# Optimization experiments

Hardware: AMD Instinct MI355X
Metric: run time of the kernel (lower is better)

The kernel has to match this reference:

```python
import jax, jax.numpy as jnp
import numpy as np

N_NODES = 50000
N_EDGES = 800000
IN_F, HID_F, OUT_F = 128, 128, 64


def setup_inputs() -> dict:
    key = jax.random.key(0)
    k1, k2, k3, k4, k5, k6 = jax.random.split(key, 6)
    edge_index = jax.random.randint(k1, (2, N_EDGES), 0, N_NODES, dtype=jnp.int64 if jax.config.jax_enable_x64 else jnp.int32)
    features = jax.random.normal(k2, (N_NODES, IN_F), dtype=jnp.float32)
    # GCNLayer weights (torch.randn init, no bias)
    W0 = jax.random.normal(k3, (IN_F, HID_F), dtype=jnp.float32)
    W1 = jax.random.normal(k4, (HID_F, HID_F), dtype=jnp.float32)
    # out_layer nn.Linear(hidden, out): weight [out, hid] used as x @ W.T + b; store transposed
    bound = 1.0 / np.sqrt(HID_F)
    W_out = jax.random.uniform(k5, (HID_F, OUT_F), minval=-bound, maxval=bound, dtype=jnp.float32)
    b_out = jax.random.uniform(k6, (OUT_F,), minval=-bound, maxval=bound, dtype=jnp.float32)
    return {"edge_index": edge_index, "features": features, "W0": W0, "W1": W1, "W_out": W_out, "b_out": b_out}


def _gcn_layer(edge_index, x, W):
    # support = x @ W ; out = A @ support ; A COO: rows=edge_index[0], cols=edge_index[1], vals=1
    support = x @ W                                   # [N, F_out]
    msgs = support[edge_index[1]]                      # gather per edge: [E, F_out]
    agg = jax.ops.segment_sum(msgs, edge_index[0], num_segments=N_NODES)  # scatter-add rows
    return jax.nn.relu(agg)


def reference(edge_index, features, W0, W1, W_out, b_out):
    x = _gcn_layer(edge_index, features, W0)
    x = _gcn_layer(edge_index, x, W1)
    return x @ W_out + b_out
```

## Files before the change

### kernel.cpp

```cpp
#include <hip/hip_runtime.h>

#define N_NODES 50000
#define N_EDGES 800000
#define SCAN_TILE 2048
#define SCAN_NBLK ((N_NODES + SCAN_TILE - 1) / SCAN_TILE)

template <int M, bool RELU_IN, bool BIAS>
__global__ __launch_bounds__(512) void gemm_k(const float* __restrict__ X,
                                              const float* __restrict__ W,
                                              const float* __restrict__ bias,
                                              float* __restrict__ Y) {
    constexpr int K = 128;
    constexpr int ROWS = 64;
    constexpr int XSTR = 136;

    __shared__ float wl[K * M];
    __shared__ float xl[ROWS * XSTR];

    const int tid = threadIdx.x;
    const int row0 = blockIdx.x * ROWS;

    {
        const float4* w4 = reinterpret_cast<const float4*>(W);
        float4* wl4 = reinterpret_cast<float4*>(wl);
        constexpr int TOT4 = K * M / 4;
        #pragma unroll
        for (int i = tid; i < TOT4; i += 512) wl4[i] = w4[i];
    }
    {
        const float4* x4 = reinterpret_cast<const float4*>(X);
        #pragma unroll
        for (int i = tid; i < ROWS * 32; i += 512) {
            const int r = i >> 5, c = i & 31;
            const int gr = row0 + r;
            float4 v = {0.f, 0.f, 0.f, 0.f};
            if (gr < N_NODES) v = x4[(size_t)gr * 32 + c];
            if (RELU_IN) {
                v.x = fmaxf(v.x, 0.f);
                v.y = fmaxf(v.y, 0.f);
                v.z = fmaxf(v.z, 0.f);
                v.w = fmaxf(v.w, 0.f);
            }
            reinterpret_cast<float4*>(&xl[r * XSTR])[c] = v;
        }
    }
    __syncthreads();

    constexpr int TPRG = M / 8;
    constexpr int NRG = 512 / TPRG;
    constexpr int TR = ROWS / NRG;
    const int rg = tid / TPRG;
    const int c0 = (tid % TPRG) * 8;

    float acc[TR][8];
    #pragma unroll
    for (int t = 0; t < TR; ++t)
        #pragma unroll
        for (int j = 0; j < 8; ++j) acc[t][j] = 0.f;

    #pragma unroll 8
    for (int k = 0; k < K; ++k) {
        const float4 wa = *reinterpret_cast<const float4*>(&wl[k * M + c0]);
        const float4 wb = *reinterpret_cast<const float4*>(&wl[k * M + c0 + 4]);
        #pragma unroll
        for (int t = 0; t < TR; ++t) {
            const float xv = xl[(rg * TR + t) * XSTR + k];
            acc[t][0] = fmaf(xv, wa.x, acc[t][0]);
            acc[t][1] = fmaf(xv, wa.y, acc[t][1]);
            acc[t][2] = fmaf(xv, wa.z, acc[t][2]);
            acc[t][3] = fmaf(xv, wa.w, acc[t][3]);
            acc[t][4] = fmaf(xv, wb.x, acc[t][4]);
            acc[t][5] = fmaf(xv, wb.y, acc[t][5]);
            acc[t][6] = fmaf(xv, wb.z, acc[t][6]);
            acc[t][7] = fmaf(xv, wb.w, acc[t][7]);
        }
    }

    #pragma unroll
    for (int t = 0; t < TR; ++t) {
        const int gr = row0 + rg * TR + t;
        if (gr >= N_NODES) continue;
        float* yp = &Y[(size_t)gr * M + c0];
        float4 o0 = {acc[t][0], acc[t][1], acc[t][2], acc[t][3]};
        float4 o1 = {acc[t][4], acc[t][5], acc[t][6], acc[t][7]};
        if (BIAS) {
            const float4 ba = *reinterpret_cast<const float4*>(&bias[c0]);
            const float4 bb = *reinterpret_cast<const float4*>(&bias[c0 + 4]);
            o0.x += ba.x; o0.y += ba.y; o0.z += ba.z; o0.w += ba.w;
            o1.x += bb.x; o1.y += bb.y; o1.z += bb.z; o1.w += bb.w;
        }
        *reinterpret_cast<float4*>(yp) = o0;
        *reinterpret_cast<float4*>(yp + 4) = o1;
    }
}

__global__ __launch_bounds__(256) void hist_k(const int* __restrict__ dst_i,
                                              int* __restrict__ cnt) {
    const int stride = gridDim.x * blockDim.x;
    for (int e = blockIdx.x * blockDim.x + threadIdx.x; e < N_EDGES; e += stride)
        atomicAdd(&cnt[dst_i[e]], 1);
}

__global__ __launch_bounds__(1024) void scan1_k(const int* __restrict__ cnt,
                                                int* __restrict__ excl,
                                                int* __restrict__ bsum) {
    __shared__ int buf[SCAN_TILE];
    const int t = threadIdx.x;
    const int base = blockIdx.x * SCAN_TILE;
    buf[t] = (base + t < N_NODES) ? cnt[base + t] : 0;
    buf[t + 1024] = (base + t + 1024 < N_NODES) ? cnt[base + t + 1024] : 0;

    for (int d = 1; d < SCAN_TILE; d <<= 1) {
        __syncthreads();
        const int idx = (t + 1) * d * 2 - 1;
        if (idx < SCAN_TILE) buf[idx] += buf[idx - d];
    }
    __syncthreads();
    if (t == 0) {
        bsum[blockIdx.x] = buf[SCAN_TILE - 1];
        buf[SCAN_TILE - 1] = 0;
    }
    for (int d = SCAN_TILE / 2; d >= 1; d >>= 1) {
        __syncthreads();
        const int idx = (t + 1) * d * 2 - 1;
        if (idx < SCAN_TILE) {
            const int tmp = buf[idx - d];
            buf[idx - d] = buf[idx];
            buf[idx] += tmp;
        }
    }
    __syncthreads();
    if (base + t < N_NODES) excl[base + t] = buf[t];
    if (base + t + 1024 < N_NODES) excl[base + t + 1024] = buf[t + 1024];
}

__global__ void scan2_k(int* __restrict__ bsum) {
    if (threadIdx.x == 0 && blockIdx.x == 0) {
        int acc = 0;
        for (int b = 0; b < SCAN_NBLK; ++b) {
            const int v = bsum[b];
            bsum[b] = acc;
            acc += v;
        }
    }
}

__global__ __launch_bounds__(256) void scan3_k(int* __restrict__ row_start,
                                               const int* __restrict__ bsum) {
    const int stride = gridDim.x * blockDim.x;
    for (int i = blockIdx.x * blockDim.x + threadIdx.x; i < N_NODES; i += stride)
        row_start[i] += bsum[i / SCAN_TILE];
    if (blockIdx.x == 0 && threadIdx.x == 0) row_start[N_NODES] = N_EDGES;
}

__global__ __launch_bounds__(256) void fill_k(const int* __restrict__ dst_i,
                                              const int* __restrict__ src_i,
                                              int* __restrict__ cursor,
                                              int* __restrict__ csr_src) {
    const int stride = gridDim.x * blockDim.x;
    for (int e = blockIdx.x * blockDim.x + threadIdx.x; e < N_EDGES; e += stride) {
        const int p = atomicAdd(&cursor[dst_i[e]], 1);
        csr_src[p] = src_i[e];
    }
}

__global__ __launch_bounds__(256) void agg_k(const float* __restrict__ S,
                                             const int* __restrict__ row_start,
                                             const int* __restrict__ csr_src,
                                             float* __restrict__ A) {
    const int wave = threadIdx.x >> 6;
    const int lane = threadIdx.x & 63;
    const int n = blockIdx.x * 4 + wave;
    if (n >= N_NODES) return;
    const int beg = row_start[n];
    const int end = row_start[n + 1];
    const float2* S2 = reinterpret_cast<const float2*>(S);

    float2 a0 = {0.f, 0.f}, a1 = {0.f, 0.f}, a2 = {0.f, 0.f}, a3 = {0.f, 0.f};
    int j = beg;
    for (; j + 3 < end; j += 4) {
        const int s0 = csr_src[j];
        const int s1 = csr_src[j + 1];
        const int s2 = csr_src[j + 2];
        const int s3 = csr_src[j + 3];
        const float2 v0 = S2[(size_t)s0 * 64 + lane];
        const float2 v1 = S2[(size_t)s1 * 64 + lane];
        const float2 v2 = S2[(size_t)s2 * 64 + lane];
        const float2 v3 = S2[(size_t)s3 * 64 + lane];
        a0.x += v0.x; a0.y += v0.y;
        a1.x += v1.x; a1.y += v1.y;
        a2.x += v2.x; a2.y += v2.y;
        a3.x += v3.x; a3.y += v3.y;
    }
    for (; j < end; ++j) {
        const int s0 = csr_src[j];
        const float2 v0 = S2[(size_t)s0 * 64 + lane];
        a0.x += v0.x; a0.y += v0.y;
    }
    a0.x += a1.x + a2.x + a3.x;
    a0.y += a1.y + a2.y + a3.y;
    reinterpret_cast<float2*>(A)[(size_t)n * 64 + lane] = a0;
}

__global__ __launch_bounds__(256) void scatter_k(const float* __restrict__ S,
                                                 const int* __restrict__ dst_i,
                                                 const int* __restrict__ src_i,
                                                 float* __restrict__ A) {
    const long total = (long)N_EDGES * 32;
    const float4* S4 = reinterpret_cast<const float4*>(S);
    const long stride = (long)gridDim.x * blockDim.x;
    for (long i = (long)blockIdx.x * blockDim.x + threadIdx.x; i < total; i += stride) {
        const int e = (int)(i >> 5);
        const int c = (int)(i & 31);
        const int s = src_i[e];
        const int d = dst_i[e];
        const float4 v = S4[(size_t)s * 32 + c];
        float* p = &A[(size_t)d * 128 + (size_t)c * 4];
        atomicAdd(p + 0, v.x);
        atomicAdd(p + 1, v.y);
        atomicAdd(p + 2, v.z);
        atomicAdd(p + 3, v.w);
    }
}

extern "C" void kernel_launch(void* const* d_in, const int* in_sizes, int n_in,
                              void* d_out, int out_size, void* d_ws, size_t ws_size,
                              hipStream_t stream) {
    const int* edge = (const int*)d_in[0];
    const float* feat = (const float*)d_in[1];
    const float* W0 = (const float*)d_in[2];
    const float* W1 = (const float*)d_in[3];
    const float* Wout = (const float*)d_in[4];
    const float* bout = (const float*)d_in[5];
    float* out = (float*)d_out;

    const int* dst_i = edge;
    const int* src_i = edge + N_EDGES;

    const size_t feat_elems = (size_t)N_NODES * 128;
    float* buf0 = (float*)d_ws;
    float* buf1 = buf0 + feat_elems;

    char* p = (char*)(buf1 + feat_elems);
    int* row_start = (int*)p;
    p += (N_NODES + 1) * sizeof(int);
    int* cursor = (int*)p;
    p += N_NODES * sizeof(int);
    int* bsum = (int*)p;
    p += 32 * sizeof(int);
    int* csr_src = (int*)p;
    p += (size_t)N_EDGES * sizeof(int);
    const size_t needed = (size_t)((char*)p - (char*)d_ws);

    const int gemm_blocks = (N_NODES + 63) / 64;
    const int agg_blocks = (N_NODES + 3) / 4;

    if (ws_size >= needed) {
        hipMemsetAsync(cursor, 0, N_NODES * sizeof(int), stream);
        hist_k<<<1024, 256, 0, stream>>>(dst_i, cursor);
        scan1_k<<<SCAN_NBLK, 1024, 0, stream>>>(cursor, row_start, bsum);
        scan2_k<<<1, 64, 0, stream>>>(bsum);
        scan3_k<<<128, 256, 0, stream>>>(row_start, bsum);
        hipMemcpyAsync(cursor, row_start, N_NODES * sizeof(int),
                       hipMemcpyDeviceToDevice, stream);
        fill_k<<<1024, 256, 0, stream>>>(dst_i, src_i, cursor, csr_src);

        gemm_k<128, false, false><<<gemm_blocks, 512, 0, stream>>>(feat, W0, nullptr, buf0);
        agg_k<<<agg_blocks, 256, 0, stream>>>(buf0, row_start, csr_src, buf1);
        gemm_k<128, true, false><<<gemm_blocks, 512, 0, stream>>>(buf1, W1, nullptr, buf0);
        agg_k<<<agg_blocks, 256, 0, stream>>>(buf0, row_start, csr_src, buf1);
        gemm_k<64, true, true><<<gemm_blocks, 512, 0, stream>>>(buf1, Wout, bout, out);
    } else {
        const size_t agg_bytes = feat_elems * sizeof(float);
        gemm_k<128, false, false><<<gemm_blocks, 512, 0, stream>>>(feat, W0, nullptr, buf0);
        hipMemsetAsync(buf1, 0, agg_bytes, stream);
        scatter_k<<<8192, 256, 0, stream>>>(buf0, dst_i, src_i, buf1);
        gemm_k<128, true, false><<<gemm_blocks, 512, 0, stream>>>(buf1, W1, nullptr, buf0);
        hipMemsetAsync(buf1, 0, agg_bytes, stream);
        scatter_k<<<8192, 256, 0, stream>>>(buf0, dst_i, src_i, buf1);
        gemm_k<64, true, true><<<gemm_blocks, 512, 0, stream>>>(buf1, Wout, bout, out);
    }
}
```

Measured before the change: 406.0 us.

## Stage GEMM weights in K-halves and merge CSR scan kernels, drop cursor copy

The GEMM now loads the weight matrix into shared memory in two K-halves, which halves the weight LDS footprint and should allow more resident blocks per CU. Columns are split into low and high quarter groups to change the LDS access pattern, at the cost of an extra barrier per half. The CSR build folds the single-thread block-sum scan into scan3 and drops the device-to-device cursor copy. Instead, fill_k advances the exclusive prefix in place so each entry ends up as the inclusive end offset, and agg reads beg and end from rs[n-1] and rs[n]. This removes two launches and a copy, though the setup kernels were a small share of total time.

New measurement: 379.0 us. 1.07x faster.

```diff
diff --git a/kernel.cpp b/kernel.cpp
--- a/kernel.cpp
+++ b/kernel.cpp
@@ -11,22 +11,16 @@
                                               const float* __restrict__ bias,
                                               float* __restrict__ Y) {
     constexpr int K = 128;
+    constexpr int KH = 64;
     constexpr int ROWS = 64;
     constexpr int XSTR = 136;
 
-    __shared__ float wl[K * M];
+    __shared__ float wl[KH * M];
     __shared__ float xl[ROWS * XSTR];
 
     const int tid = threadIdx.x;
     const int row0 = blockIdx.x * ROWS;
 
-    {
-        const float4* w4 = reinterpret_cast<const float4*>(W);
-        float4* wl4 = reinterpret_cast<float4*>(wl);
-        constexpr int TOT4 = K * M / 4;
-        #pragma unroll
-        for (int i = tid; i < TOT4; i += 512) wl4[i] = w4[i];
-    }
     {
         const float4* x4 = reinterpret_cast<const float4*>(X);
         #pragma unroll
@@ -44,13 +38,14 @@
             reinterpret_cast<float4*>(&xl[r * XSTR])[c] = v;
         }
     }
-    __syncthreads();
 
     constexpr int TPRG = M / 8;
     constexpr int NRG = 512 / TPRG;
     constexpr int TR = ROWS / NRG;
     const int rg = tid / TPRG;
-    const int c0 = (tid % TPRG) * 8;
+    const int cq = tid % TPRG;
+    const int c_lo = cq * 4;
+    const int c_hi = M / 2 + cq * 4;
 
     float acc[TR][8];
     #pragma unroll
@@ -58,39 +53,53 @@
         #pragma unroll
         for (int j = 0; j < 8; ++j) acc[t][j] = 0.f;
 
-    #pragma unroll 8
-    for (int k = 0; k < K; ++k) {
-        const float4 wa = *reinterpret_cast<const float4*>(&wl[k * M + c0]);
-        const float4 wb = *reinterpret_cast<const float4*>(&wl[k * M + c0 + 4]);
-        #pragma unroll
-        for (int t = 0; t < TR; ++t) {
-            const float xv = xl[(rg * TR + t) * XSTR + k];
-            acc[t][0] = fmaf(xv, wa.x, acc[t][0]);
-            acc[t][1] = fmaf(xv, wa.y, acc[t][1]);
-            acc[t][2] = fmaf(xv, wa.z, acc[t][2]);
-            acc[t][3] = fmaf(xv, wa.w, acc[t][3]);
-            acc[t][4] = fmaf(xv, wb.x, acc[t][4]);
-            acc[t][5] = fmaf(xv, wb.y, acc[t][5]);
-            acc[t][6] = fmaf(xv, wb.z, acc[t][6]);
-            acc[t][7] = fmaf(xv, wb.w, acc[t][7]);
-        }
+    #pragma unroll
+    for (int h = 0; h < K / KH; ++h) {
+        {
+            const float4* w4 = reinterpret_cast<const float4*>(W + h * KH * M);
+            float4* wl4 = reinterpret_cast<float4*>(wl);
+            constexpr int TOT4 = KH * M / 4;
+            #pragma unroll
+            for (int i = tid; i < TOT4; i += 512) wl4[i] = w4[i];
+        }
+        __syncthreads();
+
+        #pragma unroll 8
+        for (int k = 0; k < KH; ++k) {
+            const float4 wa = *reinterpret_cast<const float4*>(&wl[k * M + c_lo]);
+            const float4 wb = *reinterpret_cast<const float4*>(&wl[k * M + c_hi]);
+            const int gk = h * KH + k;
+            #pragma unroll
+            for (int t = 0; t < TR; ++t) {
+                const float xv = xl[(rg * TR + t) * XSTR + gk];
+                acc[t][0] = fmaf(xv, wa.x, acc[t][0]);
+                acc[t][1] = fmaf(xv, wa.y, acc[t][1]);
+                acc[t][2] = fmaf(xv, wa.z, acc[t][2]);
+                acc[t][3] = fmaf(xv, wa.w, acc[t][3]);
+                acc[t][4] = fmaf(xv, wb.x, acc[t][4]);
+                acc[t][5] = fmaf(xv, wb.y, acc[t][5]);
+                acc[t][6] = fmaf(xv, wb.z, acc[t][6]);
+                acc[t][7] = fmaf(xv, wb.w, acc[t][7]);
+            }
+        }
+        __syncthreads();
     }
 
     #pragma unroll
     for (int t = 0; t < TR; ++t) {
         const int gr = row0 + rg * TR + t;
         if (gr >= N_NODES) continue;
-        float* yp = &Y[(size_t)gr * M + c0];
+        float* yp = &Y[(size_t)gr * M];
         float4 o0 = {acc[t][0], acc[t][1], acc[t][2], acc[t][3]};
         float4 o1 = {acc[t][4], acc[t][5], acc[t][6], acc[t][7]};
         if (BIAS) {
-            const float4 ba = *reinterpret_cast<const float4*>(&bias[c0]);
-            const float4 bb = *reinterpret_cast<const float4*>(&bias[c0 + 4]);
+            const float4 ba = *reinterpret_cast<const float4*>(&bias[c_lo]);
+            const float4 bb = *reinterpret_cast<const float4*>(&bias[c_hi]);
             o0.x += ba.x; o0.y += ba.y; o0.z += ba.z; o0.w += ba.w;
             o1.x += bb.x; o1.y += bb.y; o1.z += bb.z; o1.w += bb.w;
         }
-        *reinterpret_cast<float4*>(yp) = o0;
-        *reinterpret_cast<float4*>(yp + 4) = o1;
+        *reinterpret_cast<float4*>(yp + c_lo) = o0;
+        *reinterpret_cast<float4*>(yp + c_hi) = o1;
     }
 }
 
@@ -134,46 +143,44 @@
     if (base + t + 1024 < N_NODES) excl[base + t + 1024] = buf[t + 1024];
 }
 
-__global__ void scan2_k(int* __restrict__ bsum) {
-    if (threadIdx.x == 0 && blockIdx.x == 0) {
+__global__ __launch_bounds__(256) void scan3_k(int* __restrict__ rs,
+                                               const int* __restrict__ bsum) {
+    __shared__ int pref[SCAN_NBLK];
+    if (threadIdx.x == 0) {
         int acc = 0;
+        #pragma unroll
         for (int b = 0; b < SCAN_NBLK; ++b) {
-            const int v = bsum[b];
-            bsum[b] = acc;
-            acc += v;
-        }
-    }
-}
-
-__global__ __launch_bounds__(256) void scan3_k(int* __restrict__ row_start,
-                                               const int* __restrict__ bsum) {
+            pref[b] = acc;
+            acc += bsum[b];
+        }
+    }
+    __syncthreads();
     const int stride = gridDim.x * blockDim.x;
     for (int i = blockIdx.x * blockDim.x + threadIdx.x; i < N_NODES; i += stride)
-        row_start[i] += bsum[i / SCAN_TILE];
-    if (blockIdx.x == 0 && threadIdx.x == 0) row_start[N_NODES] = N_EDGES;
+        rs[i] += pref[i / SCAN_TILE];
 }
 
 __global__ __launch_bounds__(256) void fill_k(const int* __restrict__ dst_i,
                                               const int* __restrict__ src_i,
-                                              int* __restrict__ cursor,
+                                              int* __restrict__ rs,
                                               int* __restrict__ csr_src) {
     const int stride = gridDim.x * blockDim.x;
     for (int e = blockIdx.x * blockDim.x + threadIdx.x; e < N_EDGES; e += stride) {
-        const int p = atomicAdd(&cursor[dst_i[e]], 1);
+        const int p = atomicAdd(&rs[dst_i[e]], 1);
         csr_src[p] = src_i[e];
     }
 }
 
 __global__ __launch_bounds__(256) void agg_k(const float* __restrict__ S,
-                                             const int* __restrict__ row_start,
+                                             const int* __restrict__ rs,
                                              const int* __restrict__ csr_src,
                                              float* __restrict__ A) {
     const int wave = threadIdx.x >> 6;
     const int lane = threadIdx.x & 63;
     const int n = blockIdx.x * 4 + wave;
     if (n >= N_NODES) return;
-    const int beg = row_start[n];
-    const int end = row_start[n + 1];
+    const int beg = n ? rs[n - 1] : 0;
+    const int end = rs[n];
     const float2* S2 = reinterpret_cast<const float2*>(S);
 
     float2 a0 = {0.f, 0.f}, a1 = {0.f, 0.f}, a2 = {0.f, 0.f}, a3 = {0.f, 0.f};
@@ -242,9 +249,9 @@
     float* buf1 = buf0 + feat_elems;
 
     char* p = (char*)(buf1 + feat_elems);
-    int* row_start = (int*)p;
+    int* rs = (int*)p;
     p += (N_NODES + 1) * sizeof(int);
-    int* cursor = (int*)p;
+    int* cnt = (int*)p;
     p += N_NODES * sizeof(int);
     int* bsum = (int*)p;
     p += 32 * sizeof(int);
@@ -256,19 +263,16 @@
     const int agg_blocks = (N_NODES + 3) / 4;
 
     if (ws_size >= needed) {
-        hipMemsetAsync(cursor, 0, N_NODES * sizeof(int), stream);
-        hist_k<<<1024, 256, 0, stream>>>(dst_i, cursor);
-        scan1_k<<<SCAN_NBLK, 1024, 0, stream>>>(cursor, row_start, bsum);
-        scan2_k<<<1, 64, 0, stream>>>(bsum);
-        scan3_k<<<128, 256, 0, stream>>>(row_start, bsum);
-        hipMemcpyAsync(cursor, row_start, N_NODES * sizeof(int),
-                       hipMemcpyDeviceToDevice, stream);
-        fill_k<<<1024, 256, 0, stream>>>(dst_i, src_i, cursor, csr_src);
+        hipMemsetAsync(cnt, 0, N_NODES * sizeof(int), stream);
+        hist_k<<<1024, 256, 0, stream>>>(dst_i, cnt);
+        scan1_k<<<SCAN_NBLK, 1024, 0, stream>>>(cnt, rs, bsum);
+        scan3_k<<<128, 256, 0, stream>>>(rs, bsum);
+        fill_k<<<1024, 256, 0, stream>>>(dst_i, src_i, rs, csr_src);
 
         gemm_k<128, false, false><<<gemm_blocks, 512, 0, stream>>>(feat, W0, nullptr, buf0);
-        agg_k<<<agg_blocks, 256, 0, stream>>>(buf0, row_start, csr_src, buf1);
+        agg_k<<<agg_blocks, 256, 0, stream>>>(buf0, rs, csr_src, buf1);
         gemm_k<128, true, false><<<gemm_blocks, 512, 0, stream>>>(buf1, W1, nullptr, buf0);
-        agg_k<<<agg_blocks, 256, 0, stream>>>(buf0, row_start, csr_src, buf1);
+        agg_k<<<agg_blocks, 256, 0, stream>>>(buf0, rs, csr_src, buf1);
         gemm_k<64, true, true><<<gemm_blocks, 512, 0, stream>>>(buf1, Wout, bout, out);
     } else {
         const size_t agg_bytes = feat_elems * sizeof(float);
```
